# Kernel optimization log

Measured on AMD Instinct MI355X. Metric: run time of the kernel, lower is better.

The kernel has to match this reference:

```python
import jax, jax.numpy as jnp
import numpy as np

SMOOTH = 1.0
IGNORE_INDEX = 255


def setup_inputs() -> dict:
    key = jax.random.key(0)
    k1, k2 = jax.random.split(key)
    B, C, H, W = 8, 19, 512, 512
    logits = jax.random.normal(k1, (B, C, H, W), dtype=jnp.float32)
    targets = jax.random.randint(k2, (B, H, W), 0, C, dtype=jnp.int64)
    return {"logits": logits, "targets": targets}


def reference(logits, targets):
    B, C, H, W = logits.shape
    probs = jax.nn.softmax(logits, axis=1)                      # [B,C,H,W]
    valid = targets != IGNORE_INDEX                             # [B,H,W] bool
    vf = valid.astype(probs.dtype)                              # [B,H,W]
    # clamp invalid labels to 0; their contributions are zeroed by vf
    t = jnp.where(valid, targets, 0).reshape(-1)                # [B*H*W]
    # per-class sum of probs over valid pixels (replaces boolean compaction)
    probs_sum = jnp.einsum('bchw,bhw->c', probs, vf)            # [C]
    # prob assigned to the true class at each pixel (replaces one-hot * probs)
    gathered = jnp.take_along_axis(probs, jnp.where(valid, targets, 0)[:, None], axis=1)[:, 0]  # [B,H,W]
    gathered = (gathered * vf).reshape(-1)
    intersection = jnp.zeros((C,), probs.dtype).at[t].add(gathered)   # [C]
    counts = jnp.zeros((C,), probs.dtype).at[t].add(vf.reshape(-1))   # [C] = one_hot.sum(0)
    union = probs_sum + counts
    dice = (2.0 * intersection + SMOOTH) / (union + SMOOTH)
    loss = (1.0 - dice).mean()
    # torch returns logits.sum()*0 when no valid pixels
    return jnp.where(vf.sum() > 0, loss, logits.sum() * 0.0)
```

## Files before the change

### kernel.cpp

```cpp
#include <hip/hip_runtime.h>
#include <math.h>


#define CC 19
#define HPP 131072
#define NBLK 1024
#define NTHR 256
#define NTH_TOT (NBLK * NTHR)
#define NITER 4
#define IGNORE_IDX 255

typedef float f32x2 __attribute__((ext_vector_type(2)));
typedef int   i32x2 __attribute__((ext_vector_type(2)));

__device__ __forceinline__ void issue_tile(
    f32x2 (&x)[CC], i32x2& t,
    const float* __restrict__ logits, const int* __restrict__ targets, int hq)
{
    const int b   = hq >> 17;
    const int hw2 = hq & (HPP - 1);
    const f32x2* base = (const f32x2*)logits + ((size_t)b * CC) * HPP + hw2;
#pragma unroll
    for (int c = 0; c < CC; ++c)
        x[c] = __builtin_nontemporal_load(base + (size_t)c * HPP);
    t = __builtin_nontemporal_load((const i32x2*)targets + hq);
    __builtin_amdgcn_sched_barrier(0);
}

__device__ __forceinline__ void proc_tile(
    f32x2 (&x)[CC], const i32x2 t,
    float (&accS)[CC], float (&accI)[CC], float (&accC)[CC])
{
    float s0 = 0.f, s1 = 0.f;
#pragma unroll
    for (int c = 0; c < CC; ++c) {
        x[c].x = __expf(x[c].x); s0 += x[c].x;
        x[c].y = __expf(x[c].y); s1 += x[c].y;
    }
    const float i0 = (t.x != IGNORE_IDX) ? __builtin_amdgcn_rcpf(s0) : 0.f;
    const float i1 = (t.y != IGNORE_IDX) ? __builtin_amdgcn_rcpf(s1) : 0.f;
#pragma unroll
    for (int c = 0; c < CC; ++c) {
        accS[c] = fmaf(x[c].x, i0, fmaf(x[c].y, i1, accS[c]));
        const bool h0 = (t.x == c), h1 = (t.y == c);
        accI[c] = fmaf(h0 ? x[c].x : 0.f, i0,
                  fmaf(h1 ? x[c].y : 0.f, i1, accI[c]));
        accC[c] += (h0 ? 1.f : 0.f) + (h1 ? 1.f : 0.f);
    }
}

__global__ __launch_bounds__(NTHR, 2) void dice_accum(
    const float* __restrict__ logits,
    const int* __restrict__ targets,
    float* __restrict__ sums)
{
    const int tid = blockIdx.x * NTHR + threadIdx.x;

    float accS[CC], accI[CC], accC[CC];
#pragma unroll
    for (int c = 0; c < CC; ++c) { accS[c] = 0.f; accI[c] = 0.f; accC[c] = 0.f; }

    f32x2 xa[CC], xb[CC];
    i32x2 t0, t1, t2, t3;

    issue_tile(xa, t0, logits, targets, tid);
    issue_tile(xb, t1, logits, targets, tid + NTH_TOT);
    proc_tile(xa, t0, accS, accI, accC);
    issue_tile(xa, t2, logits, targets, tid + 2 * NTH_TOT);
    proc_tile(xb, t1, accS, accI, accC);
    issue_tile(xb, t3, logits, targets, tid + 3 * NTH_TOT);
    proc_tile(xa, t2, accS, accI, accC);
    proc_tile(xb, t3, accS, accI, accC);

#pragma unroll
    for (int c = 0; c < CC; ++c) {
        for (int off = 32; off; off >>= 1) {
            accS[c] += __shfl_down(accS[c], off);
            accI[c] += __shfl_down(accI[c], off);
            accC[c] += __shfl_down(accC[c], off);
        }
    }

    __shared__ float s_part[4][64];
    const int wave = threadIdx.x >> 6;
    const int lane = threadIdx.x & 63;
    if (lane == 0) {
#pragma unroll
        for (int c = 0; c < CC; ++c) {
            s_part[wave][c]          = accS[c];
            s_part[wave][CC + c]     = accI[c];
            s_part[wave][2 * CC + c] = accC[c];
        }
    }
    __syncthreads();
    if (threadIdx.x < 3 * CC) {
        const float v = s_part[0][threadIdx.x] + s_part[1][threadIdx.x]
                      + s_part[2][threadIdx.x] + s_part[3][threadIdx.x];
        atomicAdd(&sums[threadIdx.x], v);
    }
}

__global__ __launch_bounds__(64) void dice_final(
    const float* __restrict__ sums, float* __restrict__ out)
{
    const int c = threadIdx.x;
    float term = 0.f, tv = 0.f;
    if (c < CC) {
        const float S = sums[c];
        const float I = sums[CC + c];
        const float N = sums[2 * CC + c];
        tv = N;
        term = 1.f - (2.f * I + 1.f) / (S + N + 1.f);
    }
#pragma unroll
    for (int off = 32; off; off >>= 1) {
        term += __shfl_down(term, off);
        tv   += __shfl_down(tv, off);
    }
    if (c == 0)
        out[0] = (tv > 0.f) ? term * (1.f / (float)CC) : 0.f;
}

extern "C" void kernel_launch(void* const* d_in, const int* in_sizes, int n_in,
                              void* d_out, int out_size, void* d_ws, size_t ws_size,
                              hipStream_t stream) {
    const float* logits = (const float*)d_in[0];
    const int* targets = (const int*)d_in[1];
    float* sums = (float*)d_ws;
    float* out = (float*)d_out;

    hipMemsetAsync(sums, 0, 64 * sizeof(float), stream);
    dice_accum<<<NBLK, NTHR, 0, stream>>>(logits, targets, sums);
    dice_final<<<1, 64, 0, stream>>>(sums, out);
}
```

Measured before the change: 229.4 us.

## Stage logits and targets through LDS with direct global-to-LDS loads

Replaces the per-thread register double-buffered nontemporal loads with 16-byte global_load_lds transfers. Each block stages 1024 pixels × 19 channels plus targets into shared memory, then each thread reads four pixels back from LDS and processes them. The grid is halved to 512 blocks, each looping over 4 tiles with barriers around the staging. The aim is wider, more efficient global loads. In exchange it uses about 80KB of LDS per block, which limits residency, and it loses the explicit overlap of loads with exp compute that the previous schedule had.

```diff
diff --git a/kernel.cpp b/kernel.cpp
--- a/kernel.cpp
+++ b/kernel.cpp
@@ -3,50 +3,21 @@
 
 
 #define CC 19
-#define HPP 131072
-#define NBLK 1024
+#define NBLK 512
 #define NTHR 256
-#define NTH_TOT (NBLK * NTHR)
+#define PXB 1024
 #define NITER 4
+#define PXPB 262144
 #define IGNORE_IDX 255
 
-typedef float f32x2 __attribute__((ext_vector_type(2)));
-typedef int   i32x2 __attribute__((ext_vector_type(2)));
+typedef float f32x4 __attribute__((ext_vector_type(4)));
+typedef int   i32x4 __attribute__((ext_vector_type(4)));
 
-__device__ __forceinline__ void issue_tile(
-    f32x2 (&x)[CC], i32x2& t,
-    const float* __restrict__ logits, const int* __restrict__ targets, int hq)
-{
-    const int b   = hq >> 17;
-    const int hw2 = hq & (HPP - 1);
-    const f32x2* base = (const f32x2*)logits + ((size_t)b * CC) * HPP + hw2;
-#pragma unroll
-    for (int c = 0; c < CC; ++c)
-        x[c] = __builtin_nontemporal_load(base + (size_t)c * HPP);
-    t = __builtin_nontemporal_load((const i32x2*)targets + hq);
-    __builtin_amdgcn_sched_barrier(0);
-}
-
-__device__ __forceinline__ void proc_tile(
-    f32x2 (&x)[CC], const i32x2 t,
-    float (&accS)[CC], float (&accI)[CC], float (&accC)[CC])
-{
-    float s0 = 0.f, s1 = 0.f;
-#pragma unroll
-    for (int c = 0; c < CC; ++c) {
-        x[c].x = __expf(x[c].x); s0 += x[c].x;
-        x[c].y = __expf(x[c].y); s1 += x[c].y;
-    }
-    const float i0 = (t.x != IGNORE_IDX) ? __builtin_amdgcn_rcpf(s0) : 0.f;
-    const float i1 = (t.y != IGNORE_IDX) ? __builtin_amdgcn_rcpf(s1) : 0.f;
-#pragma unroll
-    for (int c = 0; c < CC; ++c) {
-        accS[c] = fmaf(x[c].x, i0, fmaf(x[c].y, i1, accS[c]));
-        const bool h0 = (t.x == c), h1 = (t.y == c);
-        accI[c] = fmaf(h0 ? x[c].x : 0.f, i0,
-                  fmaf(h1 ? x[c].y : 0.f, i1, accI[c]));
-        accC[c] += (h0 ? 1.f : 0.f) + (h1 ? 1.f : 0.f);
-    }
+__device__ __forceinline__ void gload16(const void* g, void* l) {
+    __builtin_amdgcn_global_load_lds(
+        (const __attribute__((address_space(1))) unsigned int*)g,
+        (__attribute__((address_space(3))) unsigned int*)l,
+        16, 0, 0);
 }
 
 __global__ __launch_bounds__(NTHR, 2) void dice_accum(
@@ -54,23 +25,68 @@
     const int* __restrict__ targets,
     float* __restrict__ sums)
 {
-    const int tid = blockIdx.x * NTHR + threadIdx.x;
+    __shared__ float s_log[CC * 1024];
+    __shared__ int   s_tgt[1024];
+
+    const int wv   = threadIdx.x >> 6;
+    const int tx4  = threadIdx.x * 4;
 
     float accS[CC], accI[CC], accC[CC];
 #pragma unroll
     for (int c = 0; c < CC; ++c) { accS[c] = 0.f; accI[c] = 0.f; accC[c] = 0.f; }
 
-    f32x2 xa[CC], xb[CC];
-    i32x2 t0, t1, t2, t3;
+#pragma unroll 1
+    for (int it = 0; it < NITER; ++it) {
+        const int tile  = it * NBLK + blockIdx.x;
+        const int pxb   = tile * PXB;
+        const int batch = pxb >> 18;
+        const int hw    = pxb & (PXPB - 1);
+        const float* pbase = logits + (((size_t)(batch * CC)) << 18) + hw;
 
-    issue_tile(xa, t0, logits, targets, tid);
-    issue_tile(xb, t1, logits, targets, tid + NTH_TOT);
-    proc_tile(xa, t0, accS, accI, accC);
-    issue_tile(xa, t2, logits, targets, tid + 2 * NTH_TOT);
-    proc_tile(xb, t1, accS, accI, accC);
-    issue_tile(xb, t3, logits, targets, tid + 3 * NTH_TOT);
-    proc_tile(xa, t2, accS, accI, accC);
-    proc_tile(xb, t3, accS, accI, accC);
+#pragma unroll
+        for (int c = 0; c < CC; ++c)
+            gload16(pbase + (((size_t)c) << 18) + tx4,
+                    s_log + c * 1024 + wv * 256);
+        gload16(targets + pxb + tx4, s_tgt + wv * 256);
+
+        __syncthreads();
+
+        const i32x4 tt = ((const i32x4*)s_tgt)[threadIdx.x];
+
+        f32x4 x[CC];
+        float s0 = 0.f, s1 = 0.f, s2 = 0.f, s3 = 0.f;
+#pragma unroll
+        for (int c = 0; c < CC; ++c) {
+            f32x4 v = ((const f32x4*)s_log)[c * 256 + threadIdx.x];
+            v.x = __expf(v.x); s0 += v.x;
+            v.y = __expf(v.y); s1 += v.y;
+            v.z = __expf(v.z); s2 += v.z;
+            v.w = __expf(v.w); s3 += v.w;
+            x[c] = v;
+        }
+        const float i0 = (tt.x != IGNORE_IDX) ? __builtin_amdgcn_rcpf(s0) : 0.f;
+        const float i1 = (tt.y != IGNORE_IDX) ? __builtin_amdgcn_rcpf(s1) : 0.f;
+        const float i2 = (tt.z != IGNORE_IDX) ? __builtin_amdgcn_rcpf(s2) : 0.f;
+        const float i3 = (tt.w != IGNORE_IDX) ? __builtin_amdgcn_rcpf(s3) : 0.f;
+
+#pragma unroll
+        for (int c = 0; c < CC; ++c) {
+            accS[c] = fmaf(x[c].x, i0,
+                      fmaf(x[c].y, i1,
+                      fmaf(x[c].z, i2,
+                      fmaf(x[c].w, i3, accS[c]))));
+            const bool h0 = (tt.x == c), h1 = (tt.y == c);
+            const bool h2 = (tt.z == c), h3 = (tt.w == c);
+            accI[c] = fmaf(h0 ? x[c].x : 0.f, i0,
+                      fmaf(h1 ? x[c].y : 0.f, i1,
+                      fmaf(h2 ? x[c].z : 0.f, i2,
+                      fmaf(h3 ? x[c].w : 0.f, i3, accI[c]))));
+            accC[c] += (h0 ? 1.f : 0.f) + (h1 ? 1.f : 0.f)
+                     + (h2 ? 1.f : 0.f) + (h3 ? 1.f : 0.f);
+        }
+
+        __syncthreads();
+    }
 
 #pragma unroll
     for (int c = 0; c < CC; ++c) {
@@ -81,21 +97,20 @@
         }
     }
 
-    __shared__ float s_part[4][64];
-    const int wave = threadIdx.x >> 6;
+    float* s_part = s_log;
     const int lane = threadIdx.x & 63;
     if (lane == 0) {
 #pragma unroll
         for (int c = 0; c < CC; ++c) {
-            s_part[wave][c]          = accS[c];
-            s_part[wave][CC + c]     = accI[c];
-            s_part[wave][2 * CC + c] = accC[c];
+            s_part[wv * 64 + c]          = accS[c];
+            s_part[wv * 64 + CC + c]     = accI[c];
+            s_part[wv * 64 + 2 * CC + c] = accC[c];
         }
     }
     __syncthreads();
     if (threadIdx.x < 3 * CC) {
-        const float v = s_part[0][threadIdx.x] + s_part[1][threadIdx.x]
-                      + s_part[2][threadIdx.x] + s_part[3][threadIdx.x];
+        const float v = s_part[0 * 64 + threadIdx.x] + s_part[1 * 64 + threadIdx.x]
+                      + s_part[2 * 64 + threadIdx.x] + s_part[3 * 64 + threadIdx.x];
         atomicAdd(&sums[threadIdx.x], v);
     }
 }
```

New measurement: 229.6 us. Within noise of the previous version (+0.1%).
